# Kernel tuning notes

Measured on AMD Instinct MI355X. Metric: run time of the kernel, lower is better.

## Reference

```python
import jax, jax.numpy as jnp
import numpy as np

N_ATOMS = 8000
N_PAIRS = 80000
NF_IN = 32
NF_OUT = 32
N_DIST = 16
N_COMP = 4      # l_max=1: [l=0 (1), l=1 (3)] tensor components
N_INV = 2       # _invariant_counts[(2, 1)]
MIND_SOFT = 0.85
MAXD_SOFT = 5.0
HARD_CUTOFF = 6.5
GN_EPS = 1e-5


def _sensitivity(dist, mu, sigma):
    # HIP-NN style inverse-distance Gaussians with smooth cos^2 cutoff.
    inv_d = 1.0 / dist                                   # (P,)
    base = jnp.exp(-0.5 * ((inv_d[:, None] - mu) / sigma) ** 2)  # (P, n_dist)
    cut = jnp.where(dist < HARD_CUTOFF,
                    jnp.cos(0.5 * jnp.pi * dist / HARD_CUTOFF) ** 2, 0.0)
    return base * cut[:, None]


def setup_inputs() -> dict:
    key = jax.random.key(0)
    ks = jax.random.split(key, 10)
    in_features = jax.random.normal(ks[0], (N_ATOMS, NF_IN), jnp.float32)
    pair_first = jnp.sort(jax.random.randint(ks[1], (N_PAIRS,), 0, N_ATOMS))
    pair_second = jax.random.randint(ks[2], (N_PAIRS,), 0, N_ATOMS)
    dist_pairs = (0.5 + (HARD_CUTOFF - 0.5)
                  * jax.random.uniform(ks[3], (N_PAIRS,), jnp.float32))
    tensor_rhats = jax.random.normal(ks[4], (N_PAIRS, N_COMP), jnp.float32)
    # learned params
    sens_mu = jnp.linspace(1.0 / MAXD_SOFT, 1.0 / MIND_SOFT, N_DIST).astype(jnp.float32)
    sens_sigma = jnp.full((N_DIST,), float(sens_mu[1] - sens_mu[0]), jnp.float32)
    s_int = (2.0 / (N_DIST * NF_IN + NF_OUT)) ** 0.5
    int_weights = s_int * jax.random.normal(ks[5], (N_DIST, NF_OUT, NF_IN), jnp.float32)
    s_self = (2.0 / (NF_IN + NF_OUT)) ** 0.5
    selfint_w = s_self * jax.random.normal(ks[6], (NF_OUT, NF_IN), jnp.float32)
    selfint_b = jnp.zeros((NF_OUT,), jnp.float32)
    s_mix = (2.0 / (N_INV * NF_OUT + NF_OUT)) ** 0.5
    mixing_weights = s_mix * jax.random.normal(ks[7], (NF_OUT, N_INV, NF_OUT), jnp.float32)
    gn_weight = jnp.ones((N_INV * NF_OUT,), jnp.float32)
    gn_bias = jnp.zeros((N_INV * NF_OUT,), jnp.float32)
    return {
        "in_features": in_features, "tensor_rhats": tensor_rhats,
        "dist_pairs": dist_pairs, "int_weights": int_weights,
        "selfint_w": selfint_w, "selfint_b": selfint_b,
        "mixing_weights": mixing_weights, "gn_weight": gn_weight,
        "gn_bias": gn_bias, "sens_mu": sens_mu, "sens_sigma": sens_sigma,
        "pair_first": pair_first, "pair_second": pair_second,
    }


def reference(in_features, tensor_rhats, dist_pairs, int_weights,
              selfint_w, selfint_b, mixing_weights, gn_weight, gn_bias,
              sens_mu, sens_sigma, pair_first, pair_second):
    n_atoms = in_features.shape[0]
    # self interaction (Linear)
    self_part = in_features @ selfint_w.T + selfint_b          # (N, nf_out)
    # tensor sensitivities: (P, n_comp, n_dist) -> flat (P, n_comp*n_dist)
    sense = _sensitivity(dist_pairs, sens_mu, sens_sigma)      # (P, n_dist)
    sense_flat = (tensor_rhats[:, :, None] * sense[:, None, :]).reshape(
        -1, N_COMP * N_DIST)
    # envsum: env[a, s, f] = sum_{p: pair_first[p]=a} sense_flat[p, s] * feat[pair_second[p], f]
    feat_j = in_features[pair_second]                          # (P, nf_in)
    contrib = sense_flat[:, :, None] * feat_j[:, None, :]      # (P, S, nf_in)
    env = jax.ops.segment_sum(contrib, pair_first, num_segments=n_atoms)
    # interaction weights contraction
    w_rs = jnp.transpose(int_weights, (0, 2, 1)).reshape(N_DIST * NF_IN, NF_OUT)
    env_rs = env.reshape(n_atoms * N_COMP, N_DIST * NF_IN)
    tf = (env_rs @ w_rs).reshape(n_atoms, N_COMP, NF_OUT)
    tf = jnp.transpose(tf, (0, 2, 1))                          # (N, nf_out, n_comp)
    # HopInvariantLayer (n_max=2, l_max=1): [l=0 scalar, |l=1 vector|^2]
    invariants = jnp.stack(
        [tf[..., 0], jnp.sum(tf[..., 1:] ** 2, axis=-1)], axis=-1)  # (N, nf_out, 2)
    # GroupNorm over channels (n_inv groups of nf_out channels)
    x = jnp.transpose(invariants, (0, 2, 1))                   # (N, n_inv, nf_out)
    mean = jnp.mean(x, axis=-1, keepdims=True)
    var = jnp.var(x, axis=-1, keepdims=True)
    xn = (x - mean) / jnp.sqrt(var + GN_EPS)
    xn = xn * gn_weight.reshape(N_INV, NF_OUT) + gn_bias.reshape(N_INV, NF_OUT)
    norm_inv = jnp.transpose(xn, (0, 2, 1)).reshape(n_atoms, NF_OUT * N_INV)
    mix = norm_inv @ mixing_weights.reshape(NF_OUT * N_INV, NF_OUT)
    return mix + self_part
```

## Files before the change

kernel.cpp:

```cpp
#include <hip/hip_runtime.h>
#include <hip/hip_bf16.h>
#include <stdint.h>

#define GN_EPS 1e-5f

typedef __fp16 half2_t __attribute__((ext_vector_type(2)));
union U32H2 { uint32_t u; half2_t h; };

__device__ __forceinline__ float ldin(const void* p, int i, bool bf) {
    if (bf) {
        uint32_t u = (uint32_t)((const uint16_t*)p)[i];
        union { uint32_t u; float f; } c; c.u = u << 16;
        return c.f;
    }
    return ((const float*)p)[i];
}

__device__ __forceinline__ uint16_t f2bf(float x) {
    union { float f; uint32_t u; } c; c.f = x;
    uint32_t u = c.u;
    return (uint16_t)((u + 0x7FFFu + ((u >> 16) & 1u)) >> 16);
}

__device__ __forceinline__ bool detect_bf16(const void* gnw) {
    uint32_t det = *(const uint32_t*)gnw;
    return (det >> 16) == (det & 0xFFFFu);
}

__device__ __forceinline__ uint32_t pkh2(float lo, float hi) {
    U32H2 u; u.h = __builtin_amdgcn_cvt_pkrtz(lo, hi); return u.u;
}

#if __has_builtin(__builtin_amdgcn_fdot2)
__device__ __forceinline__ float fdot2(uint32_t a, uint32_t b, float c) {
    U32H2 ua, ub; ua.u = a; ub.u = b;
    return __builtin_amdgcn_fdot2(ua.h, ub.h, c, false);
}
#else
__device__ __forceinline__ float fdot2(uint32_t a, uint32_t b, float c) {
    U32H2 ua, ub; ua.u = a; ub.u = b;
    return c + (float)ua.h.x * (float)ub.h.x + (float)ua.h.y * (float)ub.h.y;
}
#endif

__global__ __launch_bounds__(256) void k0_prep(
    const void* __restrict__ feat, const void* __restrict__ rhats,
    const void* __restrict__ dists, const void* __restrict__ intw,
    const void* __restrict__ selfw, const void* __restrict__ selfb,
    const void* __restrict__ mw, const void* __restrict__ gnw,
    const void* __restrict__ gnb, const void* __restrict__ mu,
    const void* __restrict__ sig, const int* __restrict__ pf,
    const int* __restrict__ ps,
    int* __restrict__ seg, uint32_t* __restrict__ W2p,
    float* __restrict__ featf, float4* __restrict__ rc4,
    float2* __restrict__ dj2, float* __restrict__ mwf,
    float* __restrict__ selfwf, float* __restrict__ gnwf,
    float* __restrict__ gnbf, float* __restrict__ selfbf,
    float* __restrict__ muf, float* __restrict__ isgf,
    int n_atoms, int n_pairs)
{
    const bool bf = detect_bf16(gnw);
    const int tid = blockIdx.x * 256 + threadIdx.x;

    if (tid < n_pairs) {
        int a0 = pf[tid];
        if (tid == 0) { for (int a = 0; a <= a0; ++a) seg[a] = 0; }
        if (tid + 1 < n_pairs) {
            int a1 = pf[tid + 1];
            for (int a = a0 + 1; a <= a1; ++a) seg[a] = tid + 1;
        } else {
            for (int a = a0 + 1; a <= n_atoms; ++a) seg[a] = n_pairs;
        }
        float dist = ldin(dists, tid, bf);
        float cd = __cosf(0.2416609733530613f * dist);
        float cut = (dist < 6.5f) ? cd * cd : 0.0f;
        float4 rc;
        rc.x = ldin(rhats, 4 * tid + 0, bf) * cut;
        rc.y = ldin(rhats, 4 * tid + 1, bf) * cut;
        rc.z = ldin(rhats, 4 * tid + 2, bf) * cut;
        rc.w = ldin(rhats, 4 * tid + 3, bf) * cut;
        rc4[tid] = rc;
        float2 dj; dj.x = 1.0f / dist; dj.y = __int_as_float(ps[tid]);
        dj2[tid] = dj;
    }
    {
        int i0 = tid * 4;
#pragma unroll
        for (int k = 0; k < 4; ++k) {
            int i = i0 + k;
            if (i < n_atoms * 32) featf[i] = ldin(feat, i, bf);
        }
    }
    if (tid < 8192) {
        int o = tid & 31, fp = (tid >> 5) & 15, d = tid >> 9;
        float wlo = ldin(intw, (d * 32 + o) * 32 + 2 * fp, bf);
        float whi = ldin(intw, (d * 32 + o) * 32 + 2 * fp + 1, bf);
        W2p[tid] = pkh2(wlo, whi);
    }
    if (tid < 2048) mwf[tid] = ldin(mw, tid, bf);
    if (tid < 1024) selfwf[tid] = ldin(selfw, tid, bf);
    if (tid < 64) { gnwf[tid] = ldin(gnw, tid, bf); gnbf[tid] = ldin(gnb, tid, bf); }
    if (tid < 32) selfbf[tid] = ldin(selfb, tid, bf);
    if (tid < 16) { muf[tid] = ldin(mu, tid, bf); isgf[tid] = 1.0f / ldin(sig, tid, bf); }
}

__global__ __launch_bounds__(256, 4) void k2_main(
    const int* __restrict__ seg, const uint32_t* __restrict__ W2p,
    const float* __restrict__ featf, const float4* __restrict__ rc4,
    const float2* __restrict__ dj2, const float* __restrict__ mwf,
    const float* __restrict__ selfwf, const float* __restrict__ gnwf,
    const float* __restrict__ gnbf, const float* __restrict__ selfbf,
    const float* __restrict__ muf, const float* __restrict__ isgf,
    const void* __restrict__ gnw, void* __restrict__ out, int n_atoms)
{
    __shared__ uint32_t envs[4][1024];
    const int t = threadIdx.x, wv = t >> 6, lane = t & 63;
    const int a = blockIdx.x * 4 + wv;
    if (a >= n_atoms) return;

    const int dD = lane >> 2, fq = lane & 3;
    const float mu_d = muf[dD], isg_d = isgf[dD];

    float env[4][8];
#pragma unroll
    for (int c = 0; c < 4; ++c)
#pragma unroll
        for (int fl = 0; fl < 8; ++fl) env[c][fl] = 0.0f;

    const int s = seg[a], e = seg[a + 1];

    float4 rcN, faN, fbN; float2 djN;
    rcN = make_float4(0, 0, 0, 0); faN = rcN; fbN = rcN; djN = make_float2(1.f, 0.f);
    if (s < e) {
        rcN = rc4[s]; djN = dj2[s];
        const float4* fr = (const float4*)(featf + (size_t)__float_as_int(djN.y) * 32) + fq * 2;
        faN = fr[0]; fbN = fr[1];
    }
    for (int p = s; p < e; ++p) {
        float4 rcC = rcN, faC = faN, fbC = fbN; float2 djC = djN;
        if (p + 1 < e) {
            rcN = rc4[p + 1]; djN = dj2[p + 1];
            const float4* fr = (const float4*)(featf + (size_t)__float_as_int(djN.y) * 32) + fq * 2;
            faN = fr[0]; fbN = fr[1];
        }
        float x = (djC.x - mu_d) * isg_d;
        float sd = __expf(-0.5f * x * x);
        float t0 = sd * rcC.x, t1 = sd * rcC.y, t2 = sd * rcC.z, t3 = sd * rcC.w;
        float fj[8] = {faC.x, faC.y, faC.z, faC.w, fbC.x, fbC.y, fbC.z, fbC.w};
#pragma unroll
        for (int fl = 0; fl < 8; ++fl) {
            env[0][fl] = fmaf(t0, fj[fl], env[0][fl]);
            env[1][fl] = fmaf(t1, fj[fl], env[1][fl]);
            env[2][fl] = fmaf(t2, fj[fl], env[2][fl]);
            env[3][fl] = fmaf(t3, fj[fl], env[3][fl]);
        }
    }

    {
        int base = dD * 16 + fq * 4;
#pragma unroll
        for (int c = 0; c < 4; ++c) {
            uint4 w;
            w.x = pkh2(env[c][0], env[c][1]);
            w.y = pkh2(env[c][2], env[c][3]);
            w.z = pkh2(env[c][4], env[c][5]);
            w.w = pkh2(env[c][6], env[c][7]);
            *(uint4*)&envs[wv][c * 256 + base] = w;
        }
    }

    const int o = lane & 31, half = lane >> 5;
    const int c0 = half * 2;
    float tfA = 0.0f, tfB = 0.0f;
    {
        const uint32_t* __restrict__ wq = W2p + o;
#pragma unroll 4
        for (int dd = 0; dd < 16; ++dd) {
#pragma unroll
            for (int q4 = 0; q4 < 4; ++q4) {
                int base = dd * 16 + q4 * 4;
                uint4 eA = *(const uint4*)&envs[wv][c0 * 256 + base];
                uint4 eB = *(const uint4*)&envs[wv][(c0 + 1) * 256 + base];
                uint32_t w0 = wq[(base + 0) * 32];
                uint32_t w1 = wq[(base + 1) * 32];
                uint32_t w2 = wq[(base + 2) * 32];
                uint32_t w3 = wq[(base + 3) * 32];
                tfA = fdot2(eA.x, w0, tfA); tfA = fdot2(eA.y, w1, tfA);
                tfA = fdot2(eA.z, w2, tfA); tfA = fdot2(eA.w, w3, tfA);
                tfB = fdot2(eB.x, w0, tfB); tfB = fdot2(eB.y, w1, tfB);
                tfB = fdot2(eB.z, w2, tfB); tfB = fdot2(eB.w, w3, tfB);
            }
        }
    }

    float inv0 = __shfl(tfA, o, 64);
    float sq = (half == 0) ? tfB * tfB : fmaf(tfA, tfA, tfB * tfB);
    float inv1 = sq + __shfl_xor(sq, 32, 64);

    float s0 = inv0, q0 = inv0 * inv0, s1 = inv1, q1 = inv1 * inv1;
#pragma unroll
    for (int m = 16; m >= 1; m >>= 1) {
        s0 += __shfl_xor(s0, m, 32);
        q0 += __shfl_xor(q0, m, 32);
        s1 += __shfl_xor(s1, m, 32);
        q1 += __shfl_xor(q1, m, 32);
    }
    float mean0 = s0 * (1.f / 32.f), mean1 = s1 * (1.f / 32.f);
    float var0 = q0 * (1.f / 32.f) - mean0 * mean0;
    float var1 = q1 * (1.f / 32.f) - mean1 * mean1;
    float xn0 = (inv0 - mean0) * rsqrtf(var0 + GN_EPS);
    float xn1 = (inv1 - mean1) * rsqrtf(var1 + GN_EPS);
    xn0 = xn0 * gnwf[o] + gnbf[o];
    xn1 = xn1 * gnwf[32 + o] + gnbf[32 + o];

    float mix = 0.0f;
#pragma unroll
    for (int k = 0; k < 64; ++k) {
        float xk = __shfl((k & 1) ? xn1 : xn0, k >> 1, 32);
        mix = fmaf(xk, mwf[k * 32 + o], mix);
    }

    float sacc = selfbf[o];
    const float4* fr4 = (const float4*)(featf + (size_t)a * 32);
    const float4* sw4 = (const float4*)(selfwf + o * 32);
#pragma unroll
    for (int k = 0; k < 8; ++k) {
        float4 fv = fr4[k], w4 = sw4[k];
        sacc = fmaf(fv.x, w4.x, sacc);
        sacc = fmaf(fv.y, w4.y, sacc);
        sacc = fmaf(fv.z, w4.z, sacc);
        sacc = fmaf(fv.w, w4.w, sacc);
    }

    float res = mix + sacc;
    if (half == 0) {
        if (detect_bf16(gnw)) ((uint16_t*)out)[a * 32 + o] = f2bf(res);
        else                  ((float*)out)[a * 32 + o]    = res;
    }
}

extern "C" void kernel_launch(void* const* d_in, const int* in_sizes, int n_in,
                              void* d_out, int out_size, void* d_ws, size_t ws_size,
                              hipStream_t stream) {
    const void* feat  = d_in[0];
    const void* rhats = d_in[1];
    const void* dists = d_in[2];
    const void* intw  = d_in[3];
    const void* selfw = d_in[4];
    const void* selfb = d_in[5];
    const void* mw    = d_in[6];
    const void* gnw   = d_in[7];
    const void* gnb   = d_in[8];
    const void* mu    = d_in[9];
    const void* sig   = d_in[10];
    const int* pf     = (const int*)d_in[11];
    const int* ps     = (const int*)d_in[12];

    const int n_pairs = in_sizes[11];
    const int n_atoms = in_sizes[0] / 32;

    char* ws = (char*)d_ws;
    int*      seg    = (int*)(ws + 0);
    uint32_t* W2p    = (uint32_t*)(ws + 32768);
    float*    featf  = (float*)(ws + 65536);
    float4*   rc4    = (float4*)(ws + 1089536);
    float2*   dj2    = (float2*)(ws + 2369536);
    float*    mwf    = (float*)(ws + 3009536);
    float*    selfwf = (float*)(ws + 3017728);
    float*    gnwf   = (float*)(ws + 3021824);
    float*    gnbf   = (float*)(ws + 3022080);
    float*    selfbf = (float*)(ws + 3022336);
    float*    muf    = (float*)(ws + 3022464);
    float*    isgf   = (float*)(ws + 3022528);

    int thr = n_pairs;
    int feat_thr = (n_atoms * 32 + 3) / 4;
    if (feat_thr > thr) thr = feat_thr;
    if (thr < 8192) thr = 8192;
    hipLaunchKernelGGL(k0_prep, dim3((thr + 255) / 256), dim3(256), 0, stream,
                       feat, rhats, dists, intw, selfw, selfb, mw, gnw, gnb,
                       mu, sig, pf, ps, seg, W2p, featf, rc4, dj2, mwf,
                       selfwf, gnwf, gnbf, selfbf, muf, isgf, n_atoms, n_pairs);
    hipLaunchKernelGGL(k2_main, dim3((n_atoms + 3) / 4), dim3(256), 0, stream,
                       seg, W2p, featf, rc4, dj2, mwf, selfwf, gnwf, gnbf,
                       selfbf, muf, isgf, gnw, d_out, n_atoms);
}
```

Baseline: 126.0 us.

## Use MFMA for interaction-weight contraction and batch pair loads by four

The per-wave fdot2 contraction of env against the interaction weights is replaced by a block-level 16x16x32 f16 MFMA. The weights are repacked into MFMA-friendly order and env is stored in an XOR-swizzled shared buffer shared by all four waves, with results staged through shared memory. The pair loop now loads four pairs at a time to expose more memory parallelism than the old one-ahead prefetch. This adds two block barriers, leaves half the waves idle during the MFMA step, and keeps out-of-range waves alive so they can join the barriers.

Result: faster. 119.0 us (-5.5%).

```diff
diff --git a/kernel.cpp b/kernel.cpp
--- a/kernel.cpp
+++ b/kernel.cpp
@@ -5,7 +5,10 @@
 #define GN_EPS 1e-5f
 
 typedef __fp16 half2_t __attribute__((ext_vector_type(2)));
+typedef __fp16 v8h __attribute__((ext_vector_type(8)));
+typedef float v4f __attribute__((ext_vector_type(4)));
 union U32H2 { uint32_t u; half2_t h; };
+union U4V8 { uint4 u; v8h h; };
 
 __device__ __forceinline__ float ldin(const void* p, int i, bool bf) {
     if (bf) {
@@ -30,18 +33,6 @@
 __device__ __forceinline__ uint32_t pkh2(float lo, float hi) {
     U32H2 u; u.h = __builtin_amdgcn_cvt_pkrtz(lo, hi); return u.u;
 }
-
-#if __has_builtin(__builtin_amdgcn_fdot2)
-__device__ __forceinline__ float fdot2(uint32_t a, uint32_t b, float c) {
-    U32H2 ua, ub; ua.u = a; ub.u = b;
-    return __builtin_amdgcn_fdot2(ua.h, ub.h, c, false);
-}
-#else
-__device__ __forceinline__ float fdot2(uint32_t a, uint32_t b, float c) {
-    U32H2 ua, ub; ua.u = a; ub.u = b;
-    return c + (float)ua.h.x * (float)ub.h.x + (float)ua.h.y * (float)ub.h.y;
-}
-#endif
 
 __global__ __launch_bounds__(256) void k0_prep(
     const void* __restrict__ feat, const void* __restrict__ rhats,
@@ -51,7 +42,7 @@
     const void* __restrict__ gnb, const void* __restrict__ mu,
     const void* __restrict__ sig, const int* __restrict__ pf,
     const int* __restrict__ ps,
-    int* __restrict__ seg, uint32_t* __restrict__ W2p,
+    int* __restrict__ seg, uint32_t* __restrict__ Wmf,
     float* __restrict__ featf, float4* __restrict__ rc4,
     float2* __restrict__ dj2, float* __restrict__ mwf,
     float* __restrict__ selfwf, float* __restrict__ gnwf,
@@ -92,10 +83,10 @@
         }
     }
     if (tid < 8192) {
-        int o = tid & 31, fp = (tid >> 5) & 15, d = tid >> 9;
+        int fp = tid & 15, d = (tid >> 4) & 15, o = tid >> 8;
         float wlo = ldin(intw, (d * 32 + o) * 32 + 2 * fp, bf);
         float whi = ldin(intw, (d * 32 + o) * 32 + 2 * fp + 1, bf);
-        W2p[tid] = pkh2(wlo, whi);
+        Wmf[tid] = pkh2(wlo, whi);
     }
     if (tid < 2048) mwf[tid] = ldin(mw, tid, bf);
     if (tid < 1024) selfwf[tid] = ldin(selfw, tid, bf);
@@ -105,7 +96,7 @@
 }
 
 __global__ __launch_bounds__(256, 4) void k2_main(
-    const int* __restrict__ seg, const uint32_t* __restrict__ W2p,
+    const int* __restrict__ seg, const uint32_t* __restrict__ Wmf,
     const float* __restrict__ featf, const float4* __restrict__ rc4,
     const float2* __restrict__ dj2, const float* __restrict__ mwf,
     const float* __restrict__ selfwf, const float* __restrict__ gnwf,
@@ -113,10 +104,13 @@
     const float* __restrict__ muf, const float* __restrict__ isgf,
     const void* __restrict__ gnw, void* __restrict__ out, int n_atoms)
 {
-    __shared__ uint32_t envs[4][1024];
+    __shared__ uint32_t envs[16 * 256];
+    __shared__ float tfs[4 * 32 * 4];
+
     const int t = threadIdx.x, wv = t >> 6, lane = t & 63;
-    const int a = blockIdx.x * 4 + wv;
-    if (a >= n_atoms) return;
+    int a = blockIdx.x * 4 + wv;
+    const bool astore = (a < n_atoms);
+    if (!astore) a = n_atoms - 1;
 
     const int dD = lane >> 2, fq = lane & 3;
     const float mu_d = muf[dD], isg_d = isgf[dD];
@@ -129,73 +123,78 @@
 
     const int s = seg[a], e = seg[a + 1];
 
-    float4 rcN, faN, fbN; float2 djN;
-    rcN = make_float4(0, 0, 0, 0); faN = rcN; fbN = rcN; djN = make_float2(1.f, 0.f);
-    if (s < e) {
-        rcN = rc4[s]; djN = dj2[s];
-        const float4* fr = (const float4*)(featf + (size_t)__float_as_int(djN.y) * 32) + fq * 2;
-        faN = fr[0]; fbN = fr[1];
-    }
-    for (int p = s; p < e; ++p) {
-        float4 rcC = rcN, faC = faN, fbC = fbN; float2 djC = djN;
-        if (p + 1 < e) {
-            rcN = rc4[p + 1]; djN = dj2[p + 1];
-            const float4* fr = (const float4*)(featf + (size_t)__float_as_int(djN.y) * 32) + fq * 2;
-            faN = fr[0]; fbN = fr[1];
-        }
-        float x = (djC.x - mu_d) * isg_d;
-        float sd = __expf(-0.5f * x * x);
-        float t0 = sd * rcC.x, t1 = sd * rcC.y, t2 = sd * rcC.z, t3 = sd * rcC.w;
-        float fj[8] = {faC.x, faC.y, faC.z, faC.w, fbC.x, fbC.y, fbC.z, fbC.w};
-#pragma unroll
-        for (int fl = 0; fl < 8; ++fl) {
-            env[0][fl] = fmaf(t0, fj[fl], env[0][fl]);
-            env[1][fl] = fmaf(t1, fj[fl], env[1][fl]);
-            env[2][fl] = fmaf(t2, fj[fl], env[2][fl]);
-            env[3][fl] = fmaf(t3, fj[fl], env[3][fl]);
+    for (int p = s; p < e; p += 4) {
+        float2 dj[4]; float4 rc[4];
+#pragma unroll
+        for (int i = 0; i < 4; ++i) {
+            int pi = (p + i < e) ? p + i : e - 1;
+            dj[i] = dj2[pi];
+            float4 r = rc4[pi];
+            if (p + i >= e) r = make_float4(0.f, 0.f, 0.f, 0.f);
+            rc[i] = r;
+        }
+        float4 fa[4], fb[4];
+#pragma unroll
+        for (int i = 0; i < 4; ++i) {
+            const float4* fr = (const float4*)(featf +
+                (size_t)__float_as_int(dj[i].y) * 32) + fq * 2;
+            fa[i] = fr[0]; fb[i] = fr[1];
+        }
+#pragma unroll
+        for (int i = 0; i < 4; ++i) {
+            float x = (dj[i].x - mu_d) * isg_d;
+            float sd = __expf(-0.5f * x * x);
+            float t0 = sd * rc[i].x, t1 = sd * rc[i].y;
+            float t2 = sd * rc[i].z, t3 = sd * rc[i].w;
+            float fj[8] = {fa[i].x, fa[i].y, fa[i].z, fa[i].w,
+                           fb[i].x, fb[i].y, fb[i].z, fb[i].w};
+#pragma unroll
+            for (int fl = 0; fl < 8; ++fl) {
+                env[0][fl] = fmaf(t0, fj[fl], env[0][fl]);
+                env[1][fl] = fmaf(t1, fj[fl], env[1][fl]);
+                env[2][fl] = fmaf(t2, fj[fl], env[2][fl]);
+                env[3][fl] = fmaf(t3, fj[fl], env[3][fl]);
+            }
         }
     }
 
     {
-        int base = dD * 16 + fq * 4;
+        const int ci = dD * 4 + fq;
 #pragma unroll
         for (int c = 0; c < 4; ++c) {
+            int m = wv * 4 + c;
             uint4 w;
             w.x = pkh2(env[c][0], env[c][1]);
             w.y = pkh2(env[c][2], env[c][3]);
             w.z = pkh2(env[c][4], env[c][5]);
             w.w = pkh2(env[c][6], env[c][7]);
-            *(uint4*)&envs[wv][c * 256 + base] = w;
-        }
-    }
+            *(uint4*)&envs[m * 256 + ((ci ^ m) << 2)] = w;
+        }
+    }
+    __syncthreads();
+
+    if ((wv & 1) == 0) {
+        const int tile = wv >> 1;
+        const int mrow = lane & 15, quad = lane >> 4;
+        v4f acc = {0.f, 0.f, 0.f, 0.f};
+        const uint4* wb = (const uint4*)Wmf + ((tile * 16 + mrow) * 64 + quad);
+#pragma unroll
+        for (int kk = 0; kk < 16; ++kk) {
+            int cia = kk * 4 + quad;
+            U4V8 Af, Bf;
+            Af.u = *(const uint4*)&envs[mrow * 256 + ((cia ^ mrow) << 2)];
+            Bf.u = wb[kk * 4];
+            acc = __builtin_amdgcn_mfma_f32_16x16x32_f16(Af.h, Bf.h, acc, 0, 0, 0);
+        }
+        float4 st; st.x = acc[0]; st.y = acc[1]; st.z = acc[2]; st.w = acc[3];
+        *(float4*)&tfs[(quad * 32 + tile * 16 + mrow) * 4] = st;
+    }
+    __syncthreads();
 
     const int o = lane & 31, half = lane >> 5;
-    const int c0 = half * 2;
-    float tfA = 0.0f, tfB = 0.0f;
-    {
-        const uint32_t* __restrict__ wq = W2p + o;
-#pragma unroll 4
-        for (int dd = 0; dd < 16; ++dd) {
-#pragma unroll
-            for (int q4 = 0; q4 < 4; ++q4) {
-                int base = dd * 16 + q4 * 4;
-                uint4 eA = *(const uint4*)&envs[wv][c0 * 256 + base];
-                uint4 eB = *(const uint4*)&envs[wv][(c0 + 1) * 256 + base];
-                uint32_t w0 = wq[(base + 0) * 32];
-                uint32_t w1 = wq[(base + 1) * 32];
-                uint32_t w2 = wq[(base + 2) * 32];
-                uint32_t w3 = wq[(base + 3) * 32];
-                tfA = fdot2(eA.x, w0, tfA); tfA = fdot2(eA.y, w1, tfA);
-                tfA = fdot2(eA.z, w2, tfA); tfA = fdot2(eA.w, w3, tfA);
-                tfB = fdot2(eB.x, w0, tfB); tfB = fdot2(eB.y, w1, tfB);
-                tfB = fdot2(eB.z, w2, tfB); tfB = fdot2(eB.w, w3, tfB);
-            }
-        }
-    }
-
-    float inv0 = __shfl(tfA, o, 64);
-    float sq = (half == 0) ? tfB * tfB : fmaf(tfA, tfA, tfB * tfB);
-    float inv1 = sq + __shfl_xor(sq, 32, 64);
+    float4 tf = *(const float4*)&tfs[(wv * 32 + o) * 4];
+    float inv0 = tf.x;
+    float inv1 = tf.y * tf.y + tf.z * tf.z + tf.w * tf.w;
 
     float s0 = inv0, q0 = inv0 * inv0, s1 = inv1, q1 = inv1 * inv1;
 #pragma unroll
@@ -233,7 +232,7 @@
     }
 
     float res = mix + sacc;
-    if (half == 0) {
+    if (half == 0 && astore) {
         if (detect_bf16(gnw)) ((uint16_t*)out)[a * 32 + o] = f2bf(res);
         else                  ((float*)out)[a * 32 + o]    = res;
     }
@@ -261,7 +260,7 @@
 
     char* ws = (char*)d_ws;
     int*      seg    = (int*)(ws + 0);
-    uint32_t* W2p    = (uint32_t*)(ws + 32768);
+    uint32_t* Wmf    = (uint32_t*)(ws + 32768);
     float*    featf  = (float*)(ws + 65536);
     float4*   rc4    = (float4*)(ws + 1089536);
     float2*   dj2    = (float2*)(ws + 2369536);
@@ -279,9 +278,9 @@
     if (thr < 8192) thr = 8192;
     hipLaunchKernelGGL(k0_prep, dim3((thr + 255) / 256), dim3(256), 0, stream,
                        feat, rhats, dists, intw, selfw, selfb, mw, gnw, gnb,
-                       mu, sig, pf, ps, seg, W2p, featf, rc4, dj2, mwf,
+                       mu, sig, pf, ps, seg, Wmf, featf, rc4, dj2, mwf,
                        selfwf, gnwf, gnbf, selfbf, muf, isgf, n_atoms, n_pairs);
     hipLaunchKernelGGL(k2_main, dim3((n_atoms + 3) / 4), dim3(256), 0, stream,
-                       seg, W2p, featf, rc4, dj2, mwf, selfwf, gnwf, gnbf,
+                       seg, Wmf, featf, rc4, dj2, mwf, selfwf, gnwf, gnbf,
                        selfbf, muf, isgf, gnw, d_out, n_atoms);
 }
```
